# Kernel tuning notes

Hardware: AMD Instinct MI355X
Metric: run time of the kernel (lower is better)

Reference implementation:

```python
import jax, jax.numpy as jnp
import numpy as np

B = 2048      # env batch (graphs)
A = 8         # agents per graph (fully connected)
N = B * A     # total nodes
DIN = 192     # raw obs dim
HD = 256      # h_dim (base MLP)
MD = 256      # mem_dim (GRU)
GD = 128      # gnn_dim (per-head GATv2 out, concat=False -> head mean)
H = 4         # GAT heads
NA = 20       # n_actions
ED = 3        # edge_dim


def setup_inputs() -> dict:
    key = jax.random.key(0)
    ks = jax.random.split(key, 16)
    # fully-connected directed graph per group of A agents, no self loops
    s, d = np.meshgrid(np.arange(A), np.arange(A), indexing='ij')
    mask = s != d
    s = s[mask]; d = d[mask]                     # [A*(A-1)]
    off = (np.arange(B) * A)[:, None]
    src = (off + s[None, :]).reshape(-1)
    dst = (off + d[None, :]).reshape(-1)
    edge_index = jnp.asarray(np.stack([src, dst]), dtype=jnp.int32)  # [2, E]
    E = src.shape[0]
    p = lambda k, sh: jax.random.normal(ks[k], sh, jnp.float32) * 0.02
    return {
        'inputs': jax.random.normal(ks[0], (N, DIN), jnp.float32),
        'hidden_states': jax.random.normal(ks[1], (N, MD), jnp.float32) * 0.1,
        'edge_index': edge_index,
        'edge_attr': jax.random.uniform(ks[2], (E, ED), jnp.float32),
        # base MLP (2 layers: Linear+ReLU+LayerNorm)
        'W1': p(3, (DIN, HD)), 'b1': jnp.zeros(HD), 'g1': jnp.ones(HD), 'be1': jnp.zeros(HD),
        'W2': p(4, (HD, HD)),  'b2': jnp.zeros(HD), 'g2': jnp.ones(HD), 'be2': jnp.zeros(HD),
        # GRUCell
        'Wih': p(5, (3 * MD, HD)), 'Whh': p(6, (3 * MD, MD)),
        'bih': jnp.zeros(3 * MD), 'bhh': jnp.zeros(3 * MD),
        # GATv2Conv (edge_dim=3, heads=4, concat=False, residual)
        'Wl': p(7, (MD, H * GD)), 'bl': jnp.zeros(H * GD),
        'Wr': p(8, (MD, H * GD)), 'br': jnp.zeros(H * GD),
        'att': p(9, (H, GD)),
        'We': p(10, (ED, H * GD)),
        'Wres': p(11, (MD, GD)),
        'bg': jnp.zeros(GD),
        # head: LayerNorm + Linear
        'lng': jnp.ones(GD), 'lnb': jnp.zeros(GD),
        'Wout': p(12, (GD, NA)), 'bout': jnp.zeros(NA),
    }


def _ln(x, g, b):
    mu = jnp.mean(x, -1, keepdims=True)
    xc = x - mu
    v = jnp.mean(xc * xc, -1, keepdims=True)
    return xc * jax.lax.rsqrt(v + 1e-5) * g + b


def _fwd(inputs, hidden_states, edge_attr, edge_index,
         W1, b1, g1, be1, W2, b2, g2, be2,
         Wih, Whh, bih, bhh,
         Wl, bl, Wr, br, att, We, Wres, bg,
         lng, lnb, Wout, bout):
    src, dst = edge_index[0], edge_index[1]
    # ---- base MLP encode ----
    x = _ln(jax.nn.relu(inputs @ W1 + b1), g1, be1)
    x = _ln(jax.nn.relu(x @ W2 + b2), g2, be2)          # [N, HD]
    # ---- SimpleConv(aggr='mean', combine_root='self_loop') ----
    s = jax.ops.segment_sum(x[src], dst, num_segments=N) + x
    deg = jax.ops.segment_sum(jnp.ones(src.shape[0], x.dtype), dst, num_segments=N) + 1.0
    x = s / deg[:, None]                                 # [N, HD]
    # ---- GRUCell ----
    gi = x @ Wih.T + bih
    gh = hidden_states @ Whh.T + bhh
    ir, iz, inn = jnp.split(gi, 3, -1)
    hr, hz, hn = jnp.split(gh, 3, -1)
    r = jax.nn.sigmoid(ir + hr)
    z = jax.nn.sigmoid(iz + hz)
    n = jnp.tanh(inn + r * hn)
    h = (1.0 - z) * n + z * hidden_states                # [N, MD]
    # ---- GATv2Conv (add self loops, edge_attr fill='mean') ----
    loop = jnp.arange(N, dtype=src.dtype)
    sf = jnp.concatenate([src, loop])
    df = jnp.concatenate([dst, loop])
    ea = jnp.concatenate([edge_attr, jnp.broadcast_to(edge_attr.mean(0), (N, ED))], 0)
    xl = (h @ Wl + bl).reshape(N, H, GD)
    xr = (h @ Wr + br).reshape(N, H, GD)
    m = xl[sf] + xr[df] + (ea @ We).reshape(-1, H, GD)   # [Ef, H, GD]
    m = jnp.where(m > 0, m, 0.2 * m)                     # leaky_relu(0.2)
    logits = jnp.einsum('ehc,hc->eh', m, att)            # [Ef, H]
    mx = jax.ops.segment_max(logits, df, num_segments=N)
    ex = jnp.exp(logits - mx[df])
    den = jax.ops.segment_sum(ex, df, num_segments=N)
    alpha = ex / (den[df] + 1e-16)                       # segment softmax
    out = jax.ops.segment_sum(xl[sf] * alpha[..., None], df, num_segments=N)
    out = out.mean(1) + h @ Wres + bg                    # head mean + residual + bias
    zg = jax.nn.relu(out)                                # [N, GD]
    # ---- action head ----
    q = _ln(zg, lng, lnb) @ Wout + bout                  # [N, NA]
    return q, h


def reference(inputs, hidden_states, edge_index, edge_attr,
              W1, b1, g1, be1, W2, b2, g2, be2,
              Wih, Whh, bih, bhh,
              Wl, bl, Wr, br, att, We, Wres, bg,
              lng, lnb, Wout, bout):
    return _fwd(inputs, hidden_states, edge_attr, edge_index,
                W1, b1, g1, be1, W2, b2, g2, be2,
                Wih, Whh, bih, bhh,
                Wl, bl, Wr, br, att, We, Wres, bg,
                lng, lnb, Wout, bout)
```

## Files before the change

### kernel.cpp

```cpp
#include <hip/hip_runtime.h>
#include <hip/hip_bf16.h>

constexpr int NB  = 2048;
constexpr int AG  = 8;
constexpr int NN  = NB * AG;
constexpr int DIN = 192;
constexpr int HD  = 256;
constexpr int MD  = 256;
constexpr int GD  = 128;
constexpr int NA  = 20;
constexpr int NE  = NB * AG * (AG - 1);

typedef __attribute__((ext_vector_type(8))) short bfrag8;
typedef __attribute__((ext_vector_type(4))) short sfrag4;
typedef __attribute__((ext_vector_type(4))) float f32x4;

#define MFMA16(a, b, c) __builtin_amdgcn_mfma_f32_16x16x32_bf16((a), (b), (c), 0, 0, 0)

#define GLOAD_LDS16(g, l) __builtin_amdgcn_global_load_lds(                  \
    (const __attribute__((address_space(1))) void*)(g),                      \
    (__attribute__((address_space(3))) void*)(l), 16, 0, 0)

__device__ __forceinline__ float bf2f(__hip_bfloat16 x) { return __bfloat162float(x); }
__device__ __forceinline__ __hip_bfloat16 f2bf(float x) { return __float2bfloat16(x); }
__device__ __forceinline__ short f2bs(float x) {
    __hip_bfloat16 b = __float2bfloat16(x);
    return *reinterpret_cast<short*>(&b);
}
__device__ __forceinline__ bfrag8 ldf(const __hip_bfloat16* p) { return *(const bfrag8*)p; }
__device__ __forceinline__ bfrag8 ldf32(const float* p) {
    const f32x4 a = *(const f32x4*)p;
    const f32x4 b = *(const f32x4*)(p + 4);
    bfrag8 r;
    r[0] = f2bs(a[0]); r[1] = f2bs(a[1]); r[2] = f2bs(a[2]); r[3] = f2bs(a[3]);
    r[4] = f2bs(b[0]); r[5] = f2bs(b[1]); r[6] = f2bs(b[2]); r[7] = f2bs(b[3]);
    return r;
}
__device__ __forceinline__ float sigmf(float x) { return 1.f / (1.f + __expf(-x)); }
__device__ __forceinline__ float blo(unsigned u) { return __uint_as_float(u << 16); }
__device__ __forceinline__ float bhi(unsigned u) { return __uint_as_float(u & 0xffff0000u); }

__global__ __launch_bounds__(256) void k_prep(
    const float* __restrict__ W1, const float* __restrict__ W2,
    const float* __restrict__ Wih, const float* __restrict__ Whh,
    const float* __restrict__ Wl, const float* __restrict__ bl,
    const float* __restrict__ Wr, const float* __restrict__ br,
    const float* __restrict__ Wres, const float* __restrict__ Wout,
    const float* __restrict__ ea,
    __hip_bfloat16* __restrict__ W1T, __hip_bfloat16* __restrict__ W2T,
    __hip_bfloat16* __restrict__ WihB, __hip_bfloat16* __restrict__ WhhB,
    __hip_bfloat16* __restrict__ WcatT, float* __restrict__ WoutTf,
    float* __restrict__ bcat, float* __restrict__ ea_partials)
{
    __shared__ float sw[4][3];
    const int tid = threadIdx.x;
    if (blockIdx.x >= 3151) {
        const int b = blockIdx.x - 3151;
        float a0 = 0.f, a1 = 0.f, a2 = 0.f;
#pragma unroll
        for (int k = 0; k < 7; k++) {
            int e = b * 1792 + k * 256 + tid;
            a0 += ea[e * 3 + 0];
            a1 += ea[e * 3 + 1];
            a2 += ea[e * 3 + 2];
        }
#pragma unroll
        for (int off = 1; off < 64; off <<= 1) {
            a0 += __shfl_xor(a0, off); a1 += __shfl_xor(a1, off); a2 += __shfl_xor(a2, off);
        }
        if ((tid & 63) == 0) { sw[tid >> 6][0] = a0; sw[tid >> 6][1] = a1; sw[tid >> 6][2] = a2; }
        __syncthreads();
        if (tid == 0) {
            ea_partials[b * 3 + 0] = sw[0][0] + sw[1][0] + sw[2][0] + sw[3][0];
            ea_partials[b * 3 + 1] = sw[0][1] + sw[1][1] + sw[2][1] + sw[3][1];
            ea_partials[b * 3 + 2] = sw[0][2] + sw[1][2] + sw[2][2] + sw[3][2];
        }
        return;
    }
    int i = blockIdx.x * 256 + tid;
    if (i < 49152) { int o = i / 192, c = i % 192; W1T[i] = f2bf(W1[c * 256 + o]); return; }
    i -= 49152;
    if (i < 65536) { int o = i >> 8, c = i & 255; W2T[i] = f2bf(W2[c * 256 + o]); return; }
    i -= 65536;
    if (i < 196608) { WihB[i] = f2bf(Wih[i]); return; }
    i -= 196608;
    if (i < 196608) { WhhB[i] = f2bf(Whh[i]); return; }
    i -= 196608;
    if (i < 294912) {
        int o = i >> 8, c = i & 255;
        float v;
        if (o < 512)       v = Wl[c * 512 + o];
        else if (o < 1024) v = Wr[c * 512 + (o - 512)];
        else               v = Wres[c * 128 + (o - 1024)];
        WcatT[i] = f2bf(v); return;
    }
    i -= 294912;
    if (i < 2560) { int o = i >> 7, c = i & 127; WoutTf[i] = Wout[c * 20 + o]; return; }
    i -= 2560;
    if (i < 1152) {
        float v = 0.f;
        if (i < 512) v = bl[i]; else if (i < 1024) v = br[i - 512];
        bcat[i] = v;
    }
}

__global__ __launch_bounds__(256) void k_encode(
    const float* __restrict__ in,
    const __hip_bfloat16* __restrict__ W1T,
    const float* __restrict__ b1, const float* __restrict__ g1, const float* __restrict__ be1,
    const __hip_bfloat16* __restrict__ W2T,
    const float* __restrict__ b2, const float* __restrict__ g2, const float* __restrict__ be2,
    __hip_bfloat16* __restrict__ xm)
{
    __shared__ float sf[16][257];
    __shared__ alignas(16) __hip_bfloat16 sb[16][264];
    const int tid = threadIdx.x;
    const int lane = tid & 63, w = tid >> 6;
    const int r = lane & 15, q = lane >> 4;
    const int m0 = blockIdx.x * 16;

    {
        bfrag8 af[6];
        const float* ap = in + (size_t)(m0 + r) * DIN + q * 8;
#pragma unroll
        for (int kb = 0; kb < 6; kb++) af[kb] = ldf32(ap + kb * 32);
#pragma unroll
        for (int i = 0; i < 4; i++) {
            int t = w * 4 + i;
            const __hip_bfloat16* wp = W1T + (size_t)(t * 16 + r) * DIN + q * 8;
            bfrag8 bf[6];
#pragma unroll
            for (int kb = 0; kb < 6; kb++) bf[kb] = ldf(wp + kb * 32);
            f32x4 acc = (f32x4){0.f, 0.f, 0.f, 0.f};
#pragma unroll
            for (int kb = 0; kb < 6; kb++) acc = MFMA16(af[kb], bf[kb], acc);
            int col = t * 16 + r;
            float bias = b1[col];
#pragma unroll
            for (int reg = 0; reg < 4; reg++)
                sf[q * 4 + reg][col] = fmaxf(acc[reg] + bias, 0.f);
        }
    }
    __syncthreads();
    {
        int rowi = tid >> 4, c16 = tid & 15;
        float vals[16]; float s = 0.f, s2 = 0.f;
#pragma unroll
        for (int j = 0; j < 16; j++) { float v = sf[rowi][c16 + 16 * j]; vals[j] = v; s += v; s2 += v * v; }
#pragma unroll
        for (int off = 1; off < 16; off <<= 1) { s += __shfl_xor(s, off); s2 += __shfl_xor(s2, off); }
        float mean = s * (1.f / HD);
        float var = fmaxf(s2 * (1.f / HD) - mean * mean, 0.f);
        float rs = rsqrtf(var + 1e-5f);
#pragma unroll
        for (int j = 0; j < 16; j++) {
            int col = c16 + 16 * j;
            sb[rowi][col] = f2bf((vals[j] - mean) * rs * g1[col] + be1[col]);
        }
    }
    __syncthreads();

    {
        bfrag8 af[8];
        const __hip_bfloat16* ap = &sb[r][0];
#pragma unroll
        for (int kb = 0; kb < 8; kb++) af[kb] = ldf(ap + kb * 32 + q * 8);
        float outv[4][4];
#pragma unroll
        for (int i = 0; i < 4; i++) {
            int t = w * 4 + i;
            const __hip_bfloat16* wp = W2T + (size_t)(t * 16 + r) * HD + q * 8;
            bfrag8 bf[8];
#pragma unroll
            for (int kb = 0; kb < 8; kb++) bf[kb] = ldf(wp + kb * 32);
            f32x4 acc = (f32x4){0.f, 0.f, 0.f, 0.f};
#pragma unroll
            for (int kb = 0; kb < 8; kb++) acc = MFMA16(af[kb], bf[kb], acc);
#pragma unroll
            for (int reg = 0; reg < 4; reg++) outv[i][reg] = acc[reg];
        }
        __syncthreads();
#pragma unroll
        for (int i = 0; i < 4; i++) {
            int col = (w * 4 + i) * 16 + r;
            float bias = b2[col];
#pragma unroll
            for (int reg = 0; reg < 4; reg++)
                sf[q * 4 + reg][col] = fmaxf(outv[i][reg] + bias, 0.f);
        }
    }
    __syncthreads();
    {
        int rowi = tid >> 4, c16 = tid & 15;
        float vals[16]; float s = 0.f, s2 = 0.f;
#pragma unroll
        for (int j = 0; j < 16; j++) { float v = sf[rowi][c16 + 16 * j]; vals[j] = v; s += v; s2 += v * v; }
#pragma unroll
        for (int off = 1; off < 16; off <<= 1) { s += __shfl_xor(s, off); s2 += __shfl_xor(s2, off); }
        float mean = s * (1.f / HD);
        float var = fmaxf(s2 * (1.f / HD) - mean * mean, 0.f);
        float rs = rsqrtf(var + 1e-5f);
#pragma unroll
        for (int j = 0; j < 16; j++) {
            int col = c16 + 16 * j;
            sb[rowi][col] = f2bf((vals[j] - mean) * rs * g2[col] + be2[col]);
        }
    }
    __syncthreads();
    {
        int col = tid;
        float a0 = 0.f, a1 = 0.f;
#pragma unroll
        for (int i = 0; i < 8; i++) { a0 += bf2f(sb[i][col]); a1 += bf2f(sb[8 + i][col]); }
        xm[(size_t)(2 * blockIdx.x) * HD + col] = f2bf(a0 * 0.125f);
        xm[(size_t)(2 * blockIdx.x + 1) * HD + col] = f2bf(a1 * 0.125f);
    }
}

__global__ __launch_bounds__(256) void k_gi(
    const __hip_bfloat16* __restrict__ xm,
    const __hip_bfloat16* __restrict__ WihB,
    const float* __restrict__ bih,
    float* __restrict__ gi)
{
    const int tid = threadIdx.x;
    const int lane = tid & 63, w = tid >> 6;
    const int r = lane & 15, q = lane >> 4;
    const int m0 = (blockIdx.x >> 1) * 16;
    const int t0 = (blockIdx.x & 1) * 24;

    bfrag8 af[8];
    const __hip_bfloat16* ap = xm + (size_t)(m0 + r) * MD + q * 8;
#pragma unroll
    for (int kb = 0; kb < 8; kb++) af[kb] = ldf(ap + kb * 32);
#pragma unroll
    for (int i = 0; i < 6; i++) {
        int t = t0 + w * 6 + i;
        const __hip_bfloat16* wp = WihB + (size_t)(t * 16 + r) * MD + q * 8;
        bfrag8 bf[8];
#pragma unroll
        for (int kb = 0; kb < 8; kb++) bf[kb] = ldf(wp + kb * 32);
        f32x4 acc = (f32x4){0.f, 0.f, 0.f, 0.f};
#pragma unroll
        for (int kb = 0; kb < 8; kb++) acc = MFMA16(af[kb], bf[kb], acc);
        int col = t * 16 + r;
        float bias = bih[col];
#pragma unroll
        for (int reg = 0; reg < 4; reg++) {
            int R = m0 + q * 4 + reg;
            gi[(size_t)R * 768 + col] = acc[reg] + bias;
        }
    }
}

__global__ __launch_bounds__(256, 2) void k_gruG(
    const float* __restrict__ hprev,
    const __hip_bfloat16* __restrict__ WhhB,
    const float* __restrict__ bhh,
    const float* __restrict__ gi,
    float* __restrict__ hout)
{
    const int tid = threadIdx.x;
    const int lane = tid & 63, w = tid >> 6;
    const int r = lane & 15, q = lane >> 4;
    const int bswz = (blockIdx.x & 7) * 64 + (blockIdx.x >> 3);
    const int m0 = (bswz >> 2) * 128;
    const int cg = (bswz & 3) * 64;

    bfrag8 afr[2][8];
#pragma unroll
    for (int t = 0; t < 2; t++) {
        const float* ap = hprev + (size_t)(m0 + (w * 2 + t) * 16 + r) * MD + q * 8;
#pragma unroll
        for (int kb = 0; kb < 8; kb++) afr[t][kb] = ldf32(ap + kb * 32);
    }
    f32x4 acc[2][12];
#pragma unroll
    for (int t = 0; t < 2; t++)
#pragma unroll
        for (int n = 0; n < 12; n++) acc[t][n] = (f32x4){0.f, 0.f, 0.f, 0.f};

#pragma unroll
    for (int kb = 0; kb < 8; kb++) {
        bfrag8 bfB[12];
#pragma unroll
        for (int g = 0; g < 3; g++)
#pragma unroll
            for (int nj = 0; nj < 4; nj++)
                bfB[g * 4 + nj] = ldf(WhhB + (size_t)(g * 256 + cg + nj * 16 + r) * MD
                                      + kb * 32 + q * 8);
#pragma unroll
        for (int t = 0; t < 2; t++)
#pragma unroll
            for (int n = 0; n < 12; n++)
                acc[t][n] = MFMA16(bfB[n], afr[t][kb], acc[t][n]);
    }

#pragma unroll
    for (int t = 0; t < 2; t++) {
        int node = m0 + (w * 2 + t) * 16 + r;
        const float* gir = gi + (size_t)(node >> 3) * 768;
#pragma unroll
        for (int nj = 0; nj < 4; nj++) {
            int c = cg + nj * 16 + q * 4;
            f32x4 gR = *(const f32x4*)&gir[c];
            f32x4 gZ = *(const f32x4*)&gir[256 + c];
            f32x4 gN = *(const f32x4*)&gir[512 + c];
            f32x4 bR = *(const f32x4*)&bhh[c];
            f32x4 bZ = *(const f32x4*)&bhh[256 + c];
            f32x4 bN = *(const f32x4*)&bhh[512 + c];
            f32x4 hp = *(const f32x4*)&hprev[(size_t)node * MD + c];
            f32x4 hv;
#pragma unroll
            for (int reg = 0; reg < 4; reg++) {
                float rr = sigmf(gR[reg] + acc[t][0 + nj][reg] + bR[reg]);
                float zz = sigmf(gZ[reg] + acc[t][4 + nj][reg] + bZ[reg]);
                float nn = tanhf(gN[reg] + rr * (acc[t][8 + nj][reg] + bN[reg]));
                hv[reg] = (1.f - zz) * nn + zz * hp[reg];
            }
            *(f32x4*)&hout[(size_t)node * MD + c] = hv;
        }
    }
}

__global__ __launch_bounds__(256, 2) void k_xlr(
    const float* __restrict__ h,
    const __hip_bfloat16* __restrict__ WcatT,
    const float* __restrict__ bcat,
    __hip_bfloat16* __restrict__ xlr)
{
    __shared__ alignas(16) __hip_bfloat16 sB[128 * 64];
    const int tid = threadIdx.x;
    const int lane = tid & 63, w = tid >> 6;
    const int r = lane & 15, q = lane >> 4;
    const int wm = w >> 1, wn = w & 1;

    const int lin = (blockIdx.x & 7) * 144 + (blockIdx.x >> 3);
    const int m0 = (lin / 9) * 128;
    const int nb = (lin % 9) * 128;

    const int srow = tid >> 3;
    const int sch  = (tid & 7) ^ (srow & 7);

    f32x4 acc[4][4];
#pragma unroll
    for (int am = 0; am < 4; am++)
#pragma unroll
        for (int bn = 0; bn < 4; bn++) acc[am][bn] = (f32x4){0.f, 0.f, 0.f, 0.f};

    for (int kt = 0; kt < 4; ++kt) {
        if (kt) __syncthreads();
#pragma unroll
        for (int i = 0; i < 4; ++i) {
            const __hip_bfloat16* gp = WcatT + (size_t)(nb + i * 32 + srow) * 256
                                       + kt * 64 + sch * 8;
            GLOAD_LDS16(gp, &sB[i * 2048 + tid * 8]);
        }
        __syncthreads();

#pragma unroll
        for (int kk = 0; kk < 2; ++kk) {
            bfrag8 af[4], bf[4];
#pragma unroll
            for (int am = 0; am < 4; ++am)
                af[am] = ldf32(h + (size_t)(m0 + wm * 64 + am * 16 + r) * MD
                               + kt * 64 + kk * 32 + q * 8);
#pragma unroll
            for (int bn = 0; bn < 4; ++bn) {
                const int R = wn * 64 + bn * 16 + r;
                const int c = (kk * 4 + q) ^ (R & 7);
                bf[bn] = *(const bfrag8*)&sB[R * 64 + c * 8];
            }
#pragma unroll
            for (int am = 0; am < 4; ++am)
#pragma unroll
                for (int bn = 0; bn < 4; ++bn)
                    acc[am][bn] = MFMA16(bf[bn], af[am], acc[am][bn]);
        }
    }

#pragma unroll
    for (int bn = 0; bn < 4; ++bn) {
        const int fb = nb + wn * 64 + bn * 16 + q * 4;
        const f32x4 bv = *(const f32x4*)&bcat[fb];
#pragma unroll
        for (int am = 0; am < 4; ++am) {
            const int node = m0 + wm * 64 + am * 16 + r;
            sfrag4 pk;
#pragma unroll
            for (int reg = 0; reg < 4; reg++) pk[reg] = f2bs(acc[am][bn][reg] + bv[reg]);
            *(sfrag4*)&xlr[(size_t)node * 1152 + fb] = pk;
        }
    }
}

__global__ __launch_bounds__(256) void k_gat(
    const __hip_bfloat16* __restrict__ xlr,
    const float* __restrict__ ea,
    const float* __restrict__ ea_partials,
    const float* __restrict__ att,
    const float* __restrict__ We,
    const float* __restrict__ bg,
    const float* __restrict__ lng, const float* __restrict__ lnb,
    const float* __restrict__ WoutTf,
    const float* __restrict__ bout,
    float* __restrict__ qout)
{
    __shared__ alignas(16) char smem_raw[16 * 1160 * 2];
    __shared__ float slog[2][4][8][8];
    __shared__ float smean[4];
    __hip_bfloat16 (*sx)[1160] = (__hip_bfloat16 (*)[1160])smem_raw;
    float (*szg)[136] = (float (*)[136])smem_raw;
    const int tid = threadIdx.x;
    const int lane = tid & 63, w = tid >> 6;
    const int r = lane & 15, q = lane >> 4;
    const int m0 = blockIdx.x * 16;

    if (tid < 3) {
        float s = 0.f;
        for (int i = 0; i < 64; i++) s += ea_partials[i * 3 + tid];
        smean[tid] = s * (1.f / NE);
    }
    for (int idx = tid; idx < 2304; idx += 256) {
        int row = idx / 144, off = (idx % 144) * 8;
        *(uint4*)&sx[row][off] = *(const uint4*)&xlr[(size_t)(m0 + row) * 1152 + off];
    }

    const int sL = lane & 7, dL = lane >> 3;
    const int gg = w >> 1;
    float e0 = 0.f, e1 = 0.f, e2 = 0.f;
    if (sL != dL) {
        int eidx = sL * 7 + dL - (dL > sL ? 1 : 0);
        const float* ep = ea + (size_t)((blockIdx.x * 2 + gg) * 56 + eidx) * 3;
        e0 = ep[0]; e1 = ep[1]; e2 = ep[2];
    }
    __syncthreads();
    if (sL == dL) { e0 = smean[0]; e1 = smean[1]; e2 = smean[2]; }

    {
        const __hip_bfloat16* xlrow = &sx[gg * 8 + sL][0];
        const __hip_bfloat16* xrrow = &sx[gg * 8 + dL][512];
#pragma unroll
        for (int t = 0; t < 2; t++) {
            const int hh = (w & 1) * 2 + t;
            const int woff = __builtin_amdgcn_readfirstlane(hh * 128);
            const float* attp = att + woff;
            const float* w0p = We + woff;
            const float* w1p = We + 512 + woff;
            const float* w2p = We + 1024 + woff;
            const __hip_bfloat16* xlp = xlrow + hh * 128;
            const __hip_bfloat16* xrp = xrrow + hh * 128;
            float p0 = 0.f, p1 = 0.f;
#pragma unroll 4
            for (int cb = 0; cb < 16; cb++) {
                const uint4 uxl = *(const uint4*)&xlp[cb * 8];
                const uint4 uxr = *(const uint4*)&xrp[cb * 8];
                const f32x4 a0  = *(const f32x4*)&attp[cb * 8];
                const f32x4 a1  = *(const f32x4*)&attp[cb * 8 + 4];
                const f32x4 w00 = *(const f32x4*)&w0p[cb * 8];
                const f32x4 w01 = *(const f32x4*)&w0p[cb * 8 + 4];
                const f32x4 w10 = *(const f32x4*)&w1p[cb * 8];
                const f32x4 w11 = *(const f32x4*)&w1p[cb * 8 + 4];
                const f32x4 w20 = *(const f32x4*)&w2p[cb * 8];
                const f32x4 w21 = *(const f32x4*)&w2p[cb * 8 + 4];
                float mm;
#define CH1(XL, XR, WA, WB, WC, AT, ACC)                                          \
                mm = fmaf(e2, (WC), fmaf(e1, (WB), fmaf(e0, (WA), (XL)))) + (XR); \
                mm = fmaxf(mm, 0.2f * mm); ACC = fmaf(mm, (AT), ACC);
                CH1(blo(uxl.x), blo(uxr.x), w00[0], w10[0], w20[0], a0[0], p0)
                CH1(bhi(uxl.x), bhi(uxr.x), w00[1], w10[1], w20[1], a0[1], p1)
                CH1(blo(uxl.y), blo(uxr.y), w00[2], w10[2], w20[2], a0[2], p0)
                CH1(bhi(uxl.y), bhi(uxr.y), w00[3], w10[3], w20[3], a0[3], p1)
                CH1(blo(uxl.z), blo(uxr.z), w01[0], w11[0], w21[0], a1[0], p0)
                CH1(bhi(uxl.z), bhi(uxr.z), w01[1], w11[1], w21[1], a1[1], p1)
                CH1(blo(uxl.w), blo(uxr.w), w01[2], w11[2], w21[2], a1[2], p0)
                CH1(bhi(uxl.w), bhi(uxr.w), w01[3], w11[3], w21[3], a1[3], p1)
#undef CH1
            }
            float p = p0 + p1;
            float mx = fmaxf(p, __shfl_xor(p, 1));
            mx = fmaxf(mx, __shfl_xor(mx, 2));
            mx = fmaxf(mx, __shfl_xor(mx, 4));
            float exv = __expf(p - mx);
            float den = exv + __shfl_xor(exv, 1);
            den += __shfl_xor(den, 2);
            den += __shfl_xor(den, 4);
            ((float*)&slog[gg][hh][0][0])[lane] = exv / (den + 1e-16f);
        }
    }
    __syncthreads();

    {
        f32x4 acc0 = (f32x4){0.f, 0.f, 0.f, 0.f};
        f32x4 acc1 = (f32x4){0.f, 0.f, 0.f, 0.f};
        const int ggr = r >> 3, dr = r & 7;
#pragma unroll
        for (int ah = 0; ah < 4; ah++) {
            bfrag8 afA;
#pragma unroll
            for (int j = 0; j < 8; j++) {
                int k = q * 8 + j;
                float v = 0.f;
                if (k < 16) {
                    int ggk = k >> 3, s = k & 7;
                    if (ggk == ggr) v = slog[ggk][ah][dr][s];
                }
                afA[j] = f2bs(v);
            }
#pragma unroll
            for (int j2 = 0; j2 < 2; j2++) {
                int chunk = w * 2 + j2;
                bfrag8 bfB;
#pragma unroll
                for (int j = 0; j < 8; j++) {
                    int k = (q * 8 + j) & 15;
                    bfB[j] = *(const short*)&sx[k][ah * 128 + chunk * 16 + r];
                }
                if (j2 == 0) acc0 = MFMA16(afA, bfB, acc0);
                else         acc1 = MFMA16(afA, bfB, acc1);
            }
        }
        float ov[8];
#pragma unroll
        for (int j2 = 0; j2 < 2; j2++) {
            f32x4 a = j2 ? acc1 : acc0;
            int c = (w * 2 + j2) * 16 + r;
            float bgc = bg[c];
#pragma unroll
            for (int reg = 0; reg < 4; reg++) {
                int row = q * 4 + reg;
                float o = a[reg] * 0.25f + bf2f(sx[row][1024 + c]) + bgc;
                ov[j2 * 4 + reg] = fmaxf(o, 0.f);
            }
        }
        __syncthreads();
#pragma unroll
        for (int j2 = 0; j2 < 2; j2++) {
            int c = (w * 2 + j2) * 16 + r;
#pragma unroll
            for (int reg = 0; reg < 4; reg++)
                szg[q * 4 + reg][c] = ov[j2 * 4 + reg];
        }
    }
    __syncthreads();

    {
        int row = tid >> 4, j = tid & 15;
        float v[8]; float s = 0.f, s2 = 0.f;
#pragma unroll
        for (int cj = 0; cj < 8; cj++) { v[cj] = szg[row][j + 16 * cj]; s += v[cj]; s2 += v[cj] * v[cj]; }
#pragma unroll
        for (int off = 1; off < 16; off <<= 1) { s += __shfl_xor(s, off); s2 += __shfl_xor(s2, off); }
        float mean = s * (1.f / GD);
        float var = fmaxf(s2 * (1.f / GD) - mean * mean, 0.f);
        float rs = rsqrtf(var + 1e-5f);
#pragma unroll
        for (int cj = 0; cj < 8; cj++) {
            int c = j + 16 * cj;
            szg[row][c] = (v[cj] - mean) * rs * lng[c] + lnb[c];
        }
    }
    __syncthreads();

    {
        int row = tid >> 4, j = tid & 15;
        for (int jj = j; jj < NA; jj += 16) {
            float a = bout[jj];
            const float* wo = WoutTf + jj * 128;
#pragma unroll
            for (int c4 = 0; c4 < 32; c4++) {
                f32x4 z = *(const f32x4*)&szg[row][c4 * 4];
                const f32x4 wv = *(const f32x4*)&wo[c4 * 4];
                a = fmaf(z[0], wv[0], a); a = fmaf(z[1], wv[1], a);
                a = fmaf(z[2], wv[2], a); a = fmaf(z[3], wv[3], a);
            }
            qout[(size_t)(m0 + row) * NA + jj] = a;
        }
    }
}

extern "C" void kernel_launch(void* const* d_in, const int* in_sizes, int n_in,
                              void* d_out, int out_size, void* d_ws, size_t ws_size,
                              hipStream_t stream) {
    const float* inp   = (const float*)d_in[0];
    const float* hid   = (const float*)d_in[1];
    const float* eatt  = (const float*)d_in[3];
    const float* W1    = (const float*)d_in[4];
    const float* b1    = (const float*)d_in[5];
    const float* g1    = (const float*)d_in[6];
    const float* be1   = (const float*)d_in[7];
    const float* W2    = (const float*)d_in[8];
    const float* b2    = (const float*)d_in[9];
    const float* g2    = (const float*)d_in[10];
    const float* be2   = (const float*)d_in[11];
    const float* Wih   = (const float*)d_in[12];
    const float* Whh   = (const float*)d_in[13];
    const float* bih   = (const float*)d_in[14];
    const float* bhh   = (const float*)d_in[15];
    const float* Wl    = (const float*)d_in[16];
    const float* bl    = (const float*)d_in[17];
    const float* Wr    = (const float*)d_in[18];
    const float* br    = (const float*)d_in[19];
    const float* att   = (const float*)d_in[20];
    const float* We    = (const float*)d_in[21];
    const float* Wres  = (const float*)d_in[22];
    const float* bg    = (const float*)d_in[23];
    const float* lng   = (const float*)d_in[24];
    const float* lnb   = (const float*)d_in[25];
    const float* Wout  = (const float*)d_in[26];
    const float* bout  = (const float*)d_in[27];

    float* qout = (float*)d_out;
    float* hout = (float*)d_out + (size_t)NN * NA;

    char* ws = (char*)d_ws;
    float*           ea_partials = (float*)ws;
    __hip_bfloat16*  xm    = (__hip_bfloat16*)(ws + 2048);
    float*           gi    = (float*)(ws + 1050624);
    __hip_bfloat16*  W1T   = (__hip_bfloat16*)(ws + 7342080);
    __hip_bfloat16*  W2T   = (__hip_bfloat16*)(ws + 7440384);
    __hip_bfloat16*  WihB  = (__hip_bfloat16*)(ws + 7571456);
    __hip_bfloat16*  WhhB  = (__hip_bfloat16*)(ws + 7964672);
    __hip_bfloat16*  WcatT = (__hip_bfloat16*)(ws + 8357888);
    float*           bcat  = (float*)(ws + 8947712);
    float*           WoutTf= (float*)(ws + 8952320);
    __hip_bfloat16*  xlr   = (__hip_bfloat16*)(ws + 8962560);

    k_prep<<<3215, 256, 0, stream>>>(W1, W2, Wih, Whh, Wl, bl, Wr, br, Wres, Wout, eatt,
                                     W1T, W2T, WihB, WhhB, WcatT, WoutTf, bcat, ea_partials);
    k_encode<<<NN / 16, 256, 0, stream>>>(inp, W1T, b1, g1, be1, W2T, b2, g2, be2, xm);
    k_gi<<<256, 256, 0, stream>>>(xm, WihB, bih, gi);
    k_gruG<<<512, 256, 0, stream>>>(hid, WhhB, bhh, gi, hout);
    k_xlr<<<1152, 256, 0, stream>>>(hout, WcatT, bcat, xlr);
    k_gat<<<NN / 16, 256, 0, stream>>>(xlr, eatt, ea_partials, att, We, bg,
                                       lng, lnb, WoutTf, bout, qout);
}
```

Measured before the change: 314.3 us.

## Fuse GRU input-gate GEMM into GRU kernel and restructure GAT per graph

Removes the separate k_gi kernel. Each k_gruG block now computes its own slice of the input-gate projection (xm @ Wih) with MFMA into shared memory, which drops the fp32 gi round trip through global memory and one launch. The cost is that every column-group block recomputes the xm fragment loads. k_gat is also changed to one 8-agent graph per 128-thread block and replaces the padded MFMA attention aggregation with direct FMA over bf16 values in LDS. This cuts wasted MFMA work and LDS use but gives smaller blocks, so more blocks are launched.

```diff
diff --git a/kernel.cpp b/kernel.cpp
--- a/kernel.cpp
+++ b/kernel.cpp
@@ -217,49 +217,16 @@
     }
 }
 
-__global__ __launch_bounds__(256) void k_gi(
-    const __hip_bfloat16* __restrict__ xm,
-    const __hip_bfloat16* __restrict__ WihB,
-    const float* __restrict__ bih,
-    float* __restrict__ gi)
-{
-    const int tid = threadIdx.x;
-    const int lane = tid & 63, w = tid >> 6;
-    const int r = lane & 15, q = lane >> 4;
-    const int m0 = (blockIdx.x >> 1) * 16;
-    const int t0 = (blockIdx.x & 1) * 24;
-
-    bfrag8 af[8];
-    const __hip_bfloat16* ap = xm + (size_t)(m0 + r) * MD + q * 8;
-#pragma unroll
-    for (int kb = 0; kb < 8; kb++) af[kb] = ldf(ap + kb * 32);
-#pragma unroll
-    for (int i = 0; i < 6; i++) {
-        int t = t0 + w * 6 + i;
-        const __hip_bfloat16* wp = WihB + (size_t)(t * 16 + r) * MD + q * 8;
-        bfrag8 bf[8];
-#pragma unroll
-        for (int kb = 0; kb < 8; kb++) bf[kb] = ldf(wp + kb * 32);
-        f32x4 acc = (f32x4){0.f, 0.f, 0.f, 0.f};
-#pragma unroll
-        for (int kb = 0; kb < 8; kb++) acc = MFMA16(af[kb], bf[kb], acc);
-        int col = t * 16 + r;
-        float bias = bih[col];
-#pragma unroll
-        for (int reg = 0; reg < 4; reg++) {
-            int R = m0 + q * 4 + reg;
-            gi[(size_t)R * 768 + col] = acc[reg] + bias;
-        }
-    }
-}
-
 __global__ __launch_bounds__(256, 2) void k_gruG(
     const float* __restrict__ hprev,
     const __hip_bfloat16* __restrict__ WhhB,
     const float* __restrict__ bhh,
-    const float* __restrict__ gi,
+    const __hip_bfloat16* __restrict__ xm,
+    const __hip_bfloat16* __restrict__ WihB,
+    const float* __restrict__ bih,
     float* __restrict__ hout)
 {
+    __shared__ alignas(16) float sgi[16][200];
     const int tid = threadIdx.x;
     const int lane = tid & 63, w = tid >> 6;
     const int r = lane & 15, q = lane >> 4;
@@ -267,6 +234,31 @@
     const int m0 = (bswz >> 2) * 128;
     const int cg = (bswz & 3) * 64;
 
+    {
+        const int g0 = m0 >> 3;
+        bfrag8 axm[8];
+        const __hip_bfloat16* ap = xm + (size_t)(g0 + r) * MD + q * 8;
+#pragma unroll
+        for (int kb = 0; kb < 8; kb++) axm[kb] = ldf(ap + kb * 32);
+#pragma unroll
+        for (int i = 0; i < 3; i++) {
+            const int n = w * 3 + i;
+            const int gate = n >> 2, nj = n & 3;
+            const int colG = gate * 256 + cg + nj * 16 + r;
+            const __hip_bfloat16* wp = WihB + (size_t)colG * MD + q * 8;
+            bfrag8 bf[8];
+#pragma unroll
+            for (int kb = 0; kb < 8; kb++) bf[kb] = ldf(wp + kb * 32);
+            f32x4 acg = (f32x4){0.f, 0.f, 0.f, 0.f};
+#pragma unroll
+            for (int kb = 0; kb < 8; kb++) acg = MFMA16(axm[kb], bf[kb], acg);
+            const float bias = bih[colG];
+#pragma unroll
+            for (int reg = 0; reg < 4; reg++)
+                sgi[q * 4 + reg][n * 16 + r] = acg[reg] + bias;
+        }
+    }
+
     bfrag8 afr[2][8];
 #pragma unroll
     for (int t = 0; t < 2; t++) {
@@ -274,6 +266,8 @@
 #pragma unroll
         for (int kb = 0; kb < 8; kb++) afr[t][kb] = ldf32(ap + kb * 32);
     }
+    __syncthreads();
+
     f32x4 acc[2][12];
 #pragma unroll
     for (int t = 0; t < 2; t++)
@@ -299,13 +293,14 @@
 #pragma unroll
     for (int t = 0; t < 2; t++) {
         int node = m0 + (w * 2 + t) * 16 + r;
-        const float* gir = gi + (size_t)(node >> 3) * 768;
+        int gl = ((w * 2 + t) * 16 + r) >> 3;
 #pragma unroll
         for (int nj = 0; nj < 4; nj++) {
             int c = cg + nj * 16 + q * 4;
-            f32x4 gR = *(const f32x4*)&gir[c];
-            f32x4 gZ = *(const f32x4*)&gir[256 + c];
-            f32x4 gN = *(const f32x4*)&gir[512 + c];
+            int ci = nj * 16 + q * 4;
+            f32x4 gR = *(const f32x4*)&sgi[gl][ci];
+            f32x4 gZ = *(const f32x4*)&sgi[gl][64 + ci];
+            f32x4 gN = *(const f32x4*)&sgi[gl][128 + ci];
             f32x4 bR = *(const f32x4*)&bhh[c];
             f32x4 bZ = *(const f32x4*)&bhh[256 + c];
             f32x4 bN = *(const f32x4*)&bhh[512 + c];
@@ -394,7 +389,7 @@
     }
 }
 
-__global__ __launch_bounds__(256) void k_gat(
+__global__ __launch_bounds__(128, 4) void k_gat(
     const __hip_bfloat16* __restrict__ xlr,
     const float* __restrict__ ea,
     const float* __restrict__ ea_partials,
@@ -406,43 +401,44 @@
     const float* __restrict__ bout,
     float* __restrict__ qout)
 {
-    __shared__ alignas(16) char smem_raw[16 * 1160 * 2];
-    __shared__ float slog[2][4][8][8];
+    __shared__ alignas(16) char smem_raw[8 * 1160 * 2];
+    __shared__ float slog[4][8][8];
     __shared__ float smean[4];
     __hip_bfloat16 (*sx)[1160] = (__hip_bfloat16 (*)[1160])smem_raw;
     float (*szg)[136] = (float (*)[136])smem_raw;
     const int tid = threadIdx.x;
     const int lane = tid & 63, w = tid >> 6;
-    const int r = lane & 15, q = lane >> 4;
-    const int m0 = blockIdx.x * 16;
+    const int g = blockIdx.x;
+    const int m0 = g * 8;
 
     if (tid < 3) {
         float s = 0.f;
         for (int i = 0; i < 64; i++) s += ea_partials[i * 3 + tid];
         smean[tid] = s * (1.f / NE);
     }
-    for (int idx = tid; idx < 2304; idx += 256) {
+#pragma unroll
+    for (int k = 0; k < 9; k++) {
+        int idx = tid + k * 128;
         int row = idx / 144, off = (idx % 144) * 8;
         *(uint4*)&sx[row][off] = *(const uint4*)&xlr[(size_t)(m0 + row) * 1152 + off];
     }
 
     const int sL = lane & 7, dL = lane >> 3;
-    const int gg = w >> 1;
     float e0 = 0.f, e1 = 0.f, e2 = 0.f;
     if (sL != dL) {
         int eidx = sL * 7 + dL - (dL > sL ? 1 : 0);
-        const float* ep = ea + (size_t)((blockIdx.x * 2 + gg) * 56 + eidx) * 3;
+        const float* ep = ea + (size_t)(g * 56 + eidx) * 3;
         e0 = ep[0]; e1 = ep[1]; e2 = ep[2];
     }
     __syncthreads();
     if (sL == dL) { e0 = smean[0]; e1 = smean[1]; e2 = smean[2]; }
 
     {
-        const __hip_bfloat16* xlrow = &sx[gg * 8 + sL][0];
-        const __hip_bfloat16* xrrow = &sx[gg * 8 + dL][512];
+        const __hip_bfloat16* xlrow = &sx[sL][0];
+        const __hip_bfloat16* xrrow = &sx[dL][512];
 #pragma unroll
         for (int t = 0; t < 2; t++) {
-            const int hh = (w & 1) * 2 + t;
+            const int hh = w * 2 + t;
             const int woff = __builtin_amdgcn_readfirstlane(hh * 128);
             const float* attp = att + woff;
             const float* w0p = We + woff;
@@ -485,62 +481,45 @@
             float den = exv + __shfl_xor(exv, 1);
             den += __shfl_xor(den, 2);
             den += __shfl_xor(den, 4);
-            ((float*)&slog[gg][hh][0][0])[lane] = exv / (den + 1e-16f);
-        }
-    }
-    __syncthreads();
-
-    {
-        f32x4 acc0 = (f32x4){0.f, 0.f, 0.f, 0.f};
-        f32x4 acc1 = (f32x4){0.f, 0.f, 0.f, 0.f};
-        const int ggr = r >> 3, dr = r & 7;
-#pragma unroll
-        for (int ah = 0; ah < 4; ah++) {
-            bfrag8 afA;
-#pragma unroll
-            for (int j = 0; j < 8; j++) {
-                int k = q * 8 + j;
-                float v = 0.f;
-                if (k < 16) {
-                    int ggk = k >> 3, s = k & 7;
-                    if (ggk == ggr) v = slog[ggk][ah][dr][s];
-                }
-                afA[j] = f2bs(v);
+            ((float*)&slog[hh][0][0])[lane] = exv / (den + 1e-16f);
+        }
+    }
+    __syncthreads();
+
+    {
+        const int d = tid >> 4, cb = (tid & 15) * 8;
+        float out[8] = {0.f, 0.f, 0.f, 0.f, 0.f, 0.f, 0.f, 0.f};
+#pragma unroll
+        for (int h = 0; h < 4; h++) {
+#pragma unroll
+            for (int s = 0; s < 8; s++) {
+                const float al = slog[h][d][s];
+                const uint4 u = *(const uint4*)&sx[s][h * 128 + cb];
+                out[0] = fmaf(al, blo(u.x), out[0]);
+                out[1] = fmaf(al, bhi(u.x), out[1]);
+                out[2] = fmaf(al, blo(u.y), out[2]);
+                out[3] = fmaf(al, bhi(u.y), out[3]);
+                out[4] = fmaf(al, blo(u.z), out[4]);
+                out[5] = fmaf(al, bhi(u.z), out[5]);
+                out[6] = fmaf(al, blo(u.w), out[6]);
+                out[7] = fmaf(al, bhi(u.w), out[7]);
             }
-#pragma unroll
-            for (int j2 = 0; j2 < 2; j2++) {
-                int chunk = w * 2 + j2;
-                bfrag8 bfB;
-#pragma unroll
-                for (int j = 0; j < 8; j++) {
-                    int k = (q * 8 + j) & 15;
-                    bfB[j] = *(const short*)&sx[k][ah * 128 + chunk * 16 + r];
-                }
-                if (j2 == 0) acc0 = MFMA16(afA, bfB, acc0);
-                else         acc1 = MFMA16(afA, bfB, acc1);
-            }
-        }
-        float ov[8];
-#pragma unroll
-        for (int j2 = 0; j2 < 2; j2++) {
-            f32x4 a = j2 ? acc1 : acc0;
-            int c = (w * 2 + j2) * 16 + r;
-            float bgc = bg[c];
-#pragma unroll
-            for (int reg = 0; reg < 4; reg++) {
-                int row = q * 4 + reg;
-                float o = a[reg] * 0.25f + bf2f(sx[row][1024 + c]) + bgc;
-                ov[j2 * 4 + reg] = fmaxf(o, 0.f);
-            }
-        }
+        }
+        const uint4 ur = *(const uint4*)&sx[d][1024 + cb];
+        const f32x4 bg0 = *(const f32x4*)&bg[cb];
+        const f32x4 bg1 = *(const f32x4*)&bg[cb + 4];
+        f32x4 ov0, ov1;
+        ov0[0] = fmaxf(out[0] * 0.25f + blo(ur.x) + bg0[0], 0.f);
+        ov0[1] = fmaxf(out[1] * 0.25f + bhi(ur.x) + bg0[1], 0.f);
+        ov0[2] = fmaxf(out[2] * 0.25f + blo(ur.y) + bg0[2], 0.f);
+        ov0[3] = fmaxf(out[3] * 0.25f + bhi(ur.y) + bg0[3], 0.f);
+        ov1[0] = fmaxf(out[4] * 0.25f + blo(ur.z) + bg1[0], 0.f);
+        ov1[1] = fmaxf(out[5] * 0.25f + bhi(ur.z) + bg1[1], 0.f);
+        ov1[2] = fmaxf(out[6] * 0.25f + blo(ur.w) + bg1[2], 0.f);
+        ov1[3] = fmaxf(out[7] * 0.25f + bhi(ur.w) + bg1[3], 0.f);
         __syncthreads();
-#pragma unroll
-        for (int j2 = 0; j2 < 2; j2++) {
-            int c = (w * 2 + j2) * 16 + r;
-#pragma unroll
-            for (int reg = 0; reg < 4; reg++)
-                szg[q * 4 + reg][c] = ov[j2 * 4 + reg];
-        }
+        *(f32x4*)&szg[d][cb]     = ov0;
+        *(f32x4*)&szg[d][cb + 4] = ov1;
     }
     __syncthreads();
 
@@ -616,7 +595,6 @@
     char* ws = (char*)d_ws;
     float*           ea_partials = (float*)ws;
     __hip_bfloat16*  xm    = (__hip_bfloat16*)(ws + 2048);
-    float*           gi    = (float*)(ws + 1050624);
     __hip_bfloat16*  W1T   = (__hip_bfloat16*)(ws + 7342080);
     __hip_bfloat16*  W2T   = (__hip_bfloat16*)(ws + 7440384);
     __hip_bfloat16*  WihB  = (__hip_bfloat16*)(ws + 7571456);
@@ -629,9 +607,8 @@
     k_prep<<<3215, 256, 0, stream>>>(W1, W2, Wih, Whh, Wl, bl, Wr, br, Wres, Wout, eatt,
                                      W1T, W2T, WihB, WhhB, WcatT, WoutTf, bcat, ea_partials);
     k_encode<<<NN / 16, 256, 0, stream>>>(inp, W1T, b1, g1, be1, W2T, b2, g2, be2, xm);
-    k_gi<<<256, 256, 0, stream>>>(xm, WihB, bih, gi);
-    k_gruG<<<512, 256, 0, stream>>>(hid, WhhB, bhh, gi, hout);
+    k_gruG<<<512, 256, 0, stream>>>(hid, WhhB, bhh, xm, WihB, bih, hout);
     k_xlr<<<1152, 256, 0, stream>>>(hout, WcatT, bcat, xlr);
-    k_gat<<<NN / 16, 256, 0, stream>>>(xlr, eatt, ea_partials, att, We, bg,
-                                       lng, lnb, WoutTf, bout, qout);
-}
+    k_gat<<<NB, 128, 0, stream>>>(xlr, eatt, ea_partials, att, We, bg,
+                                  lng, lnb, WoutTf, bout, qout);
+}
```

After: 310.4 us (median of 2 runs). Within noise of the previous version (-1.2%).
